# Optimization experiments

Hardware: AMD Instinct MI355X
Metric: run time of the kernel (lower is better)

Reference implementation:

```python
import jax, jax.numpy as jnp
import numpy as np

EMBED = 1024
HEADS = 16
HEAD_DIM = EMBED // HEADS
HIDDEN = 4 * EMBED
EPS = 1e-5


def layer_norm(x, g, b):
    mu = jnp.mean(x, axis=-1, keepdims=True)
    var = jnp.var(x, axis=-1, keepdims=True)
    return (x - mu) * jax.lax.rsqrt(var + EPS) * g + b


def setup_inputs() -> dict:
    key = jax.random.key(0)
    ks = jax.random.split(key, 12)
    s_e = 1.0 / np.sqrt(EMBED)
    s_h = 1.0 / np.sqrt(HIDDEN)
    return {
        "x": jax.random.normal(ks[0], (8, 1024, EMBED), dtype=jnp.float32),
        "ln1_g": jnp.ones((EMBED,), jnp.float32),
        "ln1_b": jnp.zeros((EMBED,), jnp.float32),
        "w_qkv": jax.random.normal(ks[1], (EMBED, 3 * EMBED), jnp.float32) * s_e,
        "b_qkv": jax.random.normal(ks[2], (3 * EMBED,), jnp.float32) * s_e,
        "w_out": jax.random.normal(ks[3], (EMBED, EMBED), jnp.float32) * s_e,
        "b_out": jax.random.normal(ks[4], (EMBED,), jnp.float32) * s_e,
        "ln2_g": jnp.ones((EMBED,), jnp.float32),
        "ln2_b": jnp.zeros((EMBED,), jnp.float32),
        "w_up": jax.random.normal(ks[5], (EMBED, HIDDEN), jnp.float32) * s_e,
        "b_up": jax.random.normal(ks[6], (HIDDEN,), jnp.float32) * s_e,
        "w_down": jax.random.normal(ks[7], (HIDDEN, EMBED), jnp.float32) * s_h,
        "b_down": jax.random.normal(ks[8], (EMBED,), jnp.float32) * s_h,
    }


def reference(x, ln1_g, ln1_b, w_qkv, b_qkv, w_out, b_out,
              ln2_g, ln2_b, w_up, b_up, w_down, b_down):
    B, T, C = x.shape
    # --- attention sub-block ---
    h = layer_norm(x, ln1_g, ln1_b)
    qkv = h @ w_qkv + b_qkv                                   # [B,T,3C]
    q, k, v = jnp.split(qkv, 3, axis=-1)
    def heads(t):  # [B,T,C] -> [B,H,T,D]
        return t.reshape(B, T, HEADS, HEAD_DIM).transpose(0, 2, 1, 3)
    q, k, v = heads(q), heads(k), heads(v)
    scale = HEAD_DIM ** -0.5
    attn = jax.nn.softmax(jnp.einsum('bhqd,bhkd->bhqk', q, k) * scale, axis=-1)
    y = jnp.einsum('bhqk,bhkd->bhqd', attn, v)                # [B,H,T,D]
    y = y.transpose(0, 2, 1, 3).reshape(B, T, C)
    x = x + y @ w_out + b_out
    # --- MLP sub-block ---
    h = layer_norm(x, ln2_g, ln2_b)
    h = jax.nn.relu(h @ w_up + b_up)
    x = x + h @ w_down + b_down
    return x
```

## Files before the change

kernel.cpp:

```cpp
#include <hip/hip_runtime.h>
#include <stdint.h>


typedef __attribute__((ext_vector_type(8))) short short8;
typedef __attribute__((ext_vector_type(4))) short short4v;
typedef __attribute__((ext_vector_type(4))) float floatx4;

#define NROWS 8192

__device__ __forceinline__ unsigned short f2bf(float f) {
    union { float f; unsigned u; } x; x.f = f;
    unsigned r = x.u + 0x7fffu + ((x.u >> 16) & 1u);
    return (unsigned short)(r >> 16);
}

__device__ __forceinline__ void gl2lds16(const unsigned short* g, unsigned short* l) {
    __builtin_amdgcn_global_load_lds(
        (const __attribute__((address_space(1))) unsigned int*)(uintptr_t)g,
        (__attribute__((address_space(3))) unsigned int*)(unsigned int)(uintptr_t)l,
        16, 0, 0);
}

__global__ __launch_bounds__(256) void transpose_bf16(
    const float* __restrict__ in, unsigned short* __restrict__ out, int K, int N)
{
    __shared__ unsigned short tile[32][33];
    int n0 = blockIdx.x * 32, k0 = blockIdx.y * 32;
    int tx = threadIdx.x, ty = threadIdx.y;
    #pragma unroll
    for (int i = 0; i < 4; ++i)
        tile[ty + i * 8][tx] = f2bf(in[(size_t)(k0 + ty + i * 8) * N + n0 + tx]);
    __syncthreads();
    #pragma unroll
    for (int i = 0; i < 4; ++i)
        out[(size_t)(n0 + ty + i * 8) * K + k0 + tx] = tile[tx][ty + i * 8];
}

__global__ __launch_bounds__(256) void ln_bf16(
    const float* __restrict__ x, const float* __restrict__ g,
    const float* __restrict__ b, unsigned short* __restrict__ out)
{
    int row = blockIdx.x, t = threadIdx.x;
    const float4* xr = (const float4*)(x + (size_t)row * 1024);
    float4 v = xr[t];
    float s  = v.x + v.y + v.z + v.w;
    float s2 = v.x * v.x + v.y * v.y + v.z * v.z + v.w * v.w;
    #pragma unroll
    for (int off = 32; off; off >>= 1) {
        s  += __shfl_xor(s,  off, 64);
        s2 += __shfl_xor(s2, off, 64);
    }
    __shared__ float rs[4], rs2[4];
    int w = t >> 6;
    if ((t & 63) == 0) { rs[w] = s; rs2[w] = s2; }
    __syncthreads();
    s  = rs[0] + rs[1] + rs[2] + rs[3];
    s2 = rs2[0] + rs2[1] + rs2[2] + rs2[3];
    float mean = s * (1.0f / 1024.0f);
    float var  = s2 * (1.0f / 1024.0f) - mean * mean;
    float rstd = rsqrtf(var + 1e-5f);
    float4 gv = ((const float4*)g)[t];
    float4 bv = ((const float4*)b)[t];
    ushort4 o;
    o.x = f2bf((v.x - mean) * rstd * gv.x + bv.x);
    o.y = f2bf((v.y - mean) * rstd * gv.y + bv.y);
    o.z = f2bf((v.z - mean) * rstd * gv.z + bv.z);
    o.w = f2bf((v.w - mean) * rstd * gv.w + bv.w);
    ((ushort4*)(out + (size_t)row * 1024))[t] = o;
}

template <int MODE, int TN>
__global__ __launch_bounds__(256, 2) void gemm_mfma(
    const unsigned short* __restrict__ A, const unsigned short* __restrict__ Bt,
    int M, int N, int K,
    const float* __restrict__ bias, const float* __restrict__ resid,
    float* __restrict__ outF, unsigned short* __restrict__ outB,
    unsigned short* __restrict__ qO, unsigned short* __restrict__ kO,
    unsigned short* __restrict__ vO)
{
    constexpr int NJ  = TN / 32;
    constexpr int TNH = TN / 2;
    int m0 = blockIdx.x * 128, n0 = blockIdx.y * TN;
    int tid = threadIdx.x;
    int w = tid >> 6, l = tid & 63, quad = l >> 4, lr = l & 15;
    int wm = w & 1, wn = w >> 1;

    __shared__ unsigned short As[128 * 32];
    __shared__ unsigned short Bs[TN * 32];

    floatx4 acc[4][NJ];
    #pragma unroll
    for (int i = 0; i < 4; ++i)
        #pragma unroll
        for (int j = 0; j < NJ; ++j)
            acc[i][j] = (floatx4){0.f, 0.f, 0.f, 0.f};

    int srow = l >> 2;
    int scol = (l & 3) * 8;
    const unsigned short* Ag = A  + (size_t)(m0 + w * 32 + srow) * K + scol;
    const unsigned short* Bg = Bt + (size_t)(n0 + w * (TN / 4) + srow) * K + scol;
    unsigned short* As0 = &As[(w * 32) * 32];
    unsigned short* As1 = &As[(w * 32 + 16) * 32];
    unsigned short* Bsw = &Bs[(w * (TN / 4)) * 32];

    for (int kt = 0; kt < K; kt += 32) {
        gl2lds16(Ag + kt, As0);
        gl2lds16(Ag + (size_t)16 * K + kt, As1);
        #pragma unroll
        for (int u = 0; u < TN / 64; ++u)
            gl2lds16(Bg + (size_t)(16 * u) * K + kt, Bsw + (16 * u) * 32);
        __syncthreads();
        short8 af[4], bf[NJ];
        #pragma unroll
        for (int i = 0; i < 4; ++i)
            af[i] = *(const short8*)&As[(64 * wm + 16 * i + lr) * 32 + quad * 8];
        #pragma unroll
        for (int j = 0; j < NJ; ++j)
            bf[j] = *(const short8*)&Bs[(TNH * wn + 16 * j + lr) * 32 + quad * 8];
        #pragma unroll
        for (int i = 0; i < 4; ++i)
            #pragma unroll
            for (int j = 0; j < NJ; ++j)
                acc[i][j] = __builtin_amdgcn_mfma_f32_16x16x32_bf16(
                    af[i], bf[j], acc[i][j], 0, 0, 0);
        __syncthreads();
    }

    if (MODE == 0) {
        int sel = n0 >> 10;
        if (sel < 2) {
            const float qscale = (sel == 0) ? 0.125f : 1.0f;
            unsigned short* dst = (sel == 0) ? qO : kO;
            #pragma unroll
            for (int i = 0; i < 4; ++i)
                #pragma unroll
                for (int j = 0; j < NJ; ++j)
                    #pragma unroll
                    for (int r = 0; r < 4; ++r) {
                        int m = m0 + 64 * wm + 16 * i + quad * 4 + r;
                        int n = n0 + TNH * wn + 16 * j + lr;
                        float c = (acc[i][j][r] + bias[n]) * qscale;
                        int bb = m >> 10, t = m & 1023;
                        int cc = n & 1023, h = cc >> 6, d = cc & 63;
                        dst[(((size_t)(bb * 16 + h)) * 1024 + t) * 64 + d] = f2bf(c);
                    }
        } else {
            int bb = m0 >> 10;
            #pragma unroll
            for (int i = 0; i < 4; ++i) {
                int t0 = (m0 & 1023) + 64 * wm + 16 * i + quad * 4;
                #pragma unroll
                for (int j = 0; j < NJ; ++j) {
                    int n = n0 + TNH * wn + 16 * j + lr;
                    int cc = n & 1023, h = cc >> 6, d = cc & 63;
                    float bn = bias[n];
                    ushort4 pk;
                    pk.x = f2bf(acc[i][j][0] + bn);
                    pk.y = f2bf(acc[i][j][1] + bn);
                    pk.z = f2bf(acc[i][j][2] + bn);
                    pk.w = f2bf(acc[i][j][3] + bn);
                    *(ushort4*)&vO[((size_t)(bb * 16 + h) * 64 + d) * 1024 + t0] = pk;
                }
            }
        }
    } else {
        #pragma unroll
        for (int i = 0; i < 4; ++i)
            #pragma unroll
            for (int j = 0; j < NJ; ++j)
                #pragma unroll
                for (int r = 0; r < 4; ++r) {
                    int m = m0 + 64 * wm + 16 * i + quad * 4 + r;
                    int n = n0 + TNH * wn + 16 * j + lr;
                    float c = acc[i][j][r] + bias[n];
                    if (MODE == 1)
                        outF[(size_t)m * N + n] = c + resid[(size_t)m * N + n];
                    else
                        outB[(size_t)m * N + n] = f2bf(fmaxf(c, 0.f));
                }
    }
}

__global__ __launch_bounds__(256, 2) void attn_kernel(
    const unsigned short* __restrict__ qg, const unsigned short* __restrict__ kg,
    const unsigned short* __restrict__ vtg, unsigned short* __restrict__ y)
{
    int bid = blockIdx.x;
    int bh = bid & 127, qt = bid >> 7;
    int b = bh >> 4, h = bh & 15;
    int tid = threadIdx.x;
    int w = tid >> 6, l = tid & 63, quad = l >> 4, lr = l & 15;

    __shared__ unsigned short Qs[128 * 64];
    __shared__ unsigned short Ks[2][64 * 64];
    __shared__ unsigned short Vs[2][64 * 64];
    __shared__ unsigned short Ps[4][32 * 68];

    int srow = l >> 3;
    int scol = ((l & 7) ^ srow) * 8;

    {
        const unsigned short* qbase = qg + (size_t)bh * 65536 + (size_t)(qt * 128) * 64;
        #pragma unroll
        for (int u = 0; u < 4; ++u)
            gl2lds16(qbase + (size_t)(32 * w + 8 * u + srow) * 64 + scol,
                     &Qs[(32 * w + 8 * u) * 64]);
    }
    const unsigned short* kbase = kg  + (size_t)bh * 65536;
    const unsigned short* vbase = vtg + (size_t)bh * 65536;

    #pragma unroll
    for (int u = 0; u < 2; ++u) {
        gl2lds16(kbase + (size_t)(16 * w + 8 * u + srow) * 64 + scol,
                 &Ks[0][(16 * w + 8 * u) * 64]);
        gl2lds16(vbase + (size_t)(16 * w + 8 * u + srow) * 1024 + scol,
                 &Vs[0][(16 * w + 8 * u) * 64]);
    }
    __syncthreads();

    short8 af[2][2];
    #pragma unroll
    for (int i = 0; i < 2; ++i)
        #pragma unroll
        for (int s = 0; s < 2; ++s)
            af[i][s] = *(const short8*)
                &Qs[(32 * w + 16 * i + lr) * 64 + ((s * 4 + quad) ^ (lr & 7)) * 8];

    floatx4 o[2][4];
    float lsum[2][4];
    #pragma unroll
    for (int i = 0; i < 2; ++i)
        #pragma unroll
        for (int j = 0; j < 4; ++j) o[i][j] = (floatx4){0.f, 0.f, 0.f, 0.f};
    #pragma unroll
    for (int i = 0; i < 2; ++i)
        #pragma unroll
        for (int r = 0; r < 4; ++r) lsum[i][r] = 0.f;

    for (int kt = 0; kt < 16; ++kt) {
        int cur = kt & 1;
        if (kt + 1 < 16) {
            const unsigned short* kb = kbase + (size_t)((kt + 1) * 64) * 64;
            const unsigned short* vb = vbase + (size_t)((kt + 1) * 64);
            #pragma unroll
            for (int u = 0; u < 2; ++u) {
                gl2lds16(kb + (size_t)(16 * w + 8 * u + srow) * 64 + scol,
                         &Ks[cur ^ 1][(16 * w + 8 * u) * 64]);
                gl2lds16(vb + (size_t)(16 * w + 8 * u + srow) * 1024 + scol,
                         &Vs[cur ^ 1][(16 * w + 8 * u) * 64]);
            }
        }

        short8 kf[4][2];
        #pragma unroll
        for (int j = 0; j < 4; ++j)
            #pragma unroll
            for (int s = 0; s < 2; ++s)
                kf[j][s] = *(const short8*)
                    &Ks[cur][(16 * j + lr) * 64 + ((s * 4 + quad) ^ (lr & 7)) * 8];

        floatx4 s[2][4];
        #pragma unroll
        for (int i = 0; i < 2; ++i)
            #pragma unroll
            for (int j = 0; j < 4; ++j) {
                s[i][j] = (floatx4){0.f, 0.f, 0.f, 0.f};
                #pragma unroll
                for (int st = 0; st < 2; ++st)
                    s[i][j] = __builtin_amdgcn_mfma_f32_16x16x32_bf16(
                        af[i][st], kf[j][st], s[i][j], 0, 0, 0);
            }

        #pragma unroll
        for (int i = 0; i < 2; ++i)
            #pragma unroll
            for (int j = 0; j < 4; ++j)
                #pragma unroll
                for (int r = 0; r < 4; ++r) {
                    float p = __expf(s[i][j][r]);
                    lsum[i][r] += p;
                    Ps[w][(16 * i + quad * 4 + r) * 68 + 16 * j + lr] = f2bf(p);
                }

        asm volatile("s_waitcnt lgkmcnt(0)" ::: "memory");

        short8 vf[4][2];
        #pragma unroll
        for (int j = 0; j < 4; ++j)
            #pragma unroll
            for (int s = 0; s < 2; ++s)
                vf[j][s] = *(const short8*)
                    &Vs[cur][(16 * j + lr) * 64 + ((s * 4 + quad) ^ (lr & 7)) * 8];

        #pragma unroll
        for (int i = 0; i < 2; ++i)
            #pragma unroll
            for (int st = 0; st < 2; ++st) {
                short4v p0 = *(const short4v*)&Ps[w][(16 * i + lr) * 68 + st * 32 + quad * 8];
                short4v p1 = *(const short4v*)&Ps[w][(16 * i + lr) * 68 + st * 32 + quad * 8 + 4];
                short8 pf;
                #pragma unroll
                for (int e = 0; e < 4; ++e) { pf[e] = p0[e]; pf[e + 4] = p1[e]; }
                #pragma unroll
                for (int j = 0; j < 4; ++j)
                    o[i][j] = __builtin_amdgcn_mfma_f32_16x16x32_bf16(
                        pf, vf[j][st], o[i][j], 0, 0, 0);
            }
        __syncthreads();
    }

    #pragma unroll
    for (int off = 8; off; off >>= 1)
        #pragma unroll
        for (int i = 0; i < 2; ++i)
            #pragma unroll
            for (int r = 0; r < 4; ++r)
                lsum[i][r] += __shfl_xor(lsum[i][r], off, 64);
    float rinv[2][4];
    #pragma unroll
    for (int i = 0; i < 2; ++i)
        #pragma unroll
        for (int r = 0; r < 4; ++r) rinv[i][r] = 1.0f / lsum[i][r];

    #pragma unroll
    for (int i = 0; i < 2; ++i)
        #pragma unroll
        for (int j = 0; j < 4; ++j)
            #pragma unroll
            for (int r = 0; r < 4; ++r) {
                int trow = qt * 128 + 32 * w + 16 * i + quad * 4 + r;
                int col  = h * 64 + 16 * j + lr;
                y[((size_t)b * 1024 + trow) * 1024 + col] =
                    f2bf(o[i][j][r] * rinv[i][r]);
            }
}

extern "C" void kernel_launch(void* const* d_in, const int* in_sizes, int n_in,
                              void* d_out, int out_size, void* d_ws, size_t ws_size,
                              hipStream_t stream)
{
    const float* x      = (const float*)d_in[0];
    const float* ln1_g  = (const float*)d_in[1];
    const float* ln1_b  = (const float*)d_in[2];
    const float* w_qkv  = (const float*)d_in[3];
    const float* b_qkv  = (const float*)d_in[4];
    const float* w_out  = (const float*)d_in[5];
    const float* b_out  = (const float*)d_in[6];
    const float* ln2_g  = (const float*)d_in[7];
    const float* ln2_b  = (const float*)d_in[8];
    const float* w_up   = (const float*)d_in[9];
    const float* b_up   = (const float*)d_in[10];
    const float* w_down = (const float*)d_in[11];
    const float* b_down = (const float*)d_in[12];

    char* ws = (char*)d_ws;
    unsigned short* wqkvT  = (unsigned short*)(ws + 0);
    unsigned short* woutT  = (unsigned short*)(ws + 6291456);
    unsigned short* wupT   = (unsigned short*)(ws + 8388608);
    unsigned short* wdownT = (unsigned short*)(ws + 16777216);
    float*          x2     = (float*)(ws + 25165824);
    unsigned short* h1     = (unsigned short*)(ws + 58720256);
    unsigned short* qb     = (unsigned short*)(ws + 75497472);
    unsigned short* kb     = (unsigned short*)(ws + 92274688);
    unsigned short* vtb    = (unsigned short*)(ws + 109051904);
    unsigned short* yb     = (unsigned short*)(ws + 125829120);
    unsigned short* a2     = (unsigned short*)(ws + 75497472);
    unsigned short* h2     = h1;

    transpose_bf16<<<dim3(3072 / 32, 1024 / 32), dim3(32, 8), 0, stream>>>(w_qkv, wqkvT, 1024, 3072);
    transpose_bf16<<<dim3(1024 / 32, 1024 / 32), dim3(32, 8), 0, stream>>>(w_out, woutT, 1024, 1024);
    transpose_bf16<<<dim3(4096 / 32, 1024 / 32), dim3(32, 8), 0, stream>>>(w_up,  wupT,  1024, 4096);
    transpose_bf16<<<dim3(1024 / 32, 4096 / 32), dim3(32, 8), 0, stream>>>(w_down, wdownT, 4096, 1024);

    ln_bf16<<<NROWS, 256, 0, stream>>>(x, ln1_g, ln1_b, h1);

    gemm_mfma<0, 256><<<dim3(NROWS / 128, 3072 / 256), 256, 0, stream>>>(
        h1, wqkvT, NROWS, 3072, 1024, b_qkv, nullptr, nullptr, nullptr, qb, kb, vtb);

    attn_kernel<<<1024, 256, 0, stream>>>(qb, kb, vtb, yb);

    gemm_mfma<1, 128><<<dim3(NROWS / 128, 1024 / 128), 256, 0, stream>>>(
        yb, woutT, NROWS, 1024, 1024, b_out, x, x2, nullptr, nullptr, nullptr, nullptr);

    ln_bf16<<<NROWS, 256, 0, stream>>>(x2, ln2_g, ln2_b, h2);

    gemm_mfma<2, 256><<<dim3(NROWS / 128, 4096 / 256), 256, 0, stream>>>(
        h2, wupT, NROWS, 4096, 1024, b_up, nullptr, nullptr, a2, nullptr, nullptr, nullptr);

    gemm_mfma<1, 128><<<dim3(NROWS / 128, 1024 / 128), 256, 0, stream>>>(
        a2, wdownT, NROWS, 1024, 4096, b_down, x2, (float*)d_out, nullptr, nullptr, nullptr, nullptr);
}
```

Measured before the change: 490.4 us.

## Add double-buffered swizzled-LDS GEMM for residual projections

Adds a new gemm_dbuf kernel for the out-projection and down-projection GEMMs. It uses K-tiles of 64, double-buffered LDS so the next tile's global-to-LDS loads overlap MFMA work, and an XOR swizzle on LDS columns to avoid bank conflicts. There is one barrier per iteration instead of two. The LDS footprint grows to 64KB per block, which may limit occupancy. The old templated GEMM is specialised to TN=256 for the QKV and up projections.

```diff
diff --git a/kernel.cpp b/kernel.cpp
--- a/kernel.cpp
+++ b/kernel.cpp
@@ -69,17 +69,98 @@
     ((ushort4*)(out + (size_t)row * 1024))[t] = o;
 }
 
-template <int MODE, int TN>
+__global__ __launch_bounds__(256, 2) void gemm_dbuf(
+    const unsigned short* __restrict__ A, const unsigned short* __restrict__ Bt,
+    int M, int N, int K,
+    const float* __restrict__ bias, const float* __restrict__ resid,
+    float* __restrict__ outF)
+{
+    int m0 = blockIdx.x * 128, n0 = blockIdx.y * 128;
+    int tid = threadIdx.x;
+    int w = tid >> 6, l = tid & 63, quad = l >> 4, lr = l & 15;
+    int wm = w & 1, wn = w >> 1;
+
+    __shared__ unsigned short As[2][128 * 64];
+    __shared__ unsigned short Bs[2][128 * 64];
+
+    floatx4 acc[4][4];
+    #pragma unroll
+    for (int i = 0; i < 4; ++i)
+        #pragma unroll
+        for (int j = 0; j < 4; ++j)
+            acc[i][j] = (floatx4){0.f, 0.f, 0.f, 0.f};
+
+    int srow = l >> 3;
+    int scol = ((l & 7) ^ srow) * 8;
+    const unsigned short* Ag = A  + (size_t)(m0 + 32 * w + srow) * K + scol;
+    const unsigned short* Bg = Bt + (size_t)(n0 + 32 * w + srow) * K + scol;
+
+    #pragma unroll
+    for (int u = 0; u < 4; ++u) {
+        gl2lds16(Ag + (size_t)(8 * u) * K, &As[0][(32 * w + 8 * u) * 64]);
+        gl2lds16(Bg + (size_t)(8 * u) * K, &Bs[0][(32 * w + 8 * u) * 64]);
+    }
+    __syncthreads();
+
+    for (int kt = 0; kt < K; kt += 64) {
+        int cur = (kt >> 6) & 1;
+        if (kt + 64 < K) {
+            #pragma unroll
+            for (int u = 0; u < 4; ++u) {
+                gl2lds16(Ag + (size_t)(8 * u) * K + kt + 64,
+                         &As[cur ^ 1][(32 * w + 8 * u) * 64]);
+                gl2lds16(Bg + (size_t)(8 * u) * K + kt + 64,
+                         &Bs[cur ^ 1][(32 * w + 8 * u) * 64]);
+            }
+        }
+        short8 af[4][2], bf[4][2];
+        #pragma unroll
+        for (int i = 0; i < 4; ++i)
+            #pragma unroll
+            for (int s = 0; s < 2; ++s)
+                af[i][s] = *(const short8*)
+                    &As[cur][(64 * wm + 16 * i + lr) * 64 + (((s * 4 + quad) ^ (lr & 7)) * 8)];
+        #pragma unroll
+        for (int j = 0; j < 4; ++j)
+            #pragma unroll
+            for (int s = 0; s < 2; ++s)
+                bf[j][s] = *(const short8*)
+                    &Bs[cur][(64 * wn + 16 * j + lr) * 64 + (((s * 4 + quad) ^ (lr & 7)) * 8)];
+        #pragma unroll
+        for (int i = 0; i < 4; ++i)
+            #pragma unroll
+            for (int j = 0; j < 4; ++j) {
+                acc[i][j] = __builtin_amdgcn_mfma_f32_16x16x32_bf16(
+                    af[i][0], bf[j][0], acc[i][j], 0, 0, 0);
+                acc[i][j] = __builtin_amdgcn_mfma_f32_16x16x32_bf16(
+                    af[i][1], bf[j][1], acc[i][j], 0, 0, 0);
+            }
+        __syncthreads();
+    }
+
+    #pragma unroll
+    for (int i = 0; i < 4; ++i)
+        #pragma unroll
+        for (int j = 0; j < 4; ++j)
+            #pragma unroll
+            for (int r = 0; r < 4; ++r) {
+                int m = m0 + 64 * wm + 16 * i + quad * 4 + r;
+                int n = n0 + 64 * wn + 16 * j + lr;
+                outF[(size_t)m * N + n] =
+                    acc[i][j][r] + bias[n] + resid[(size_t)m * N + n];
+            }
+}
+
+template <int MODE>
 __global__ __launch_bounds__(256, 2) void gemm_mfma(
     const unsigned short* __restrict__ A, const unsigned short* __restrict__ Bt,
     int M, int N, int K,
-    const float* __restrict__ bias, const float* __restrict__ resid,
-    float* __restrict__ outF, unsigned short* __restrict__ outB,
+    const float* __restrict__ bias,
+    unsigned short* __restrict__ outB,
     unsigned short* __restrict__ qO, unsigned short* __restrict__ kO,
     unsigned short* __restrict__ vO)
 {
-    constexpr int NJ  = TN / 32;
-    constexpr int TNH = TN / 2;
+    constexpr int TN = 256, NJ = 8, TNH = 128;
     int m0 = blockIdx.x * 128, n0 = blockIdx.y * TN;
     int tid = threadIdx.x;
     int w = tid >> 6, l = tid & 63, quad = l >> 4, lr = l & 15;
@@ -98,16 +179,16 @@
     int srow = l >> 2;
     int scol = (l & 3) * 8;
     const unsigned short* Ag = A  + (size_t)(m0 + w * 32 + srow) * K + scol;
-    const unsigned short* Bg = Bt + (size_t)(n0 + w * (TN / 4) + srow) * K + scol;
+    const unsigned short* Bg = Bt + (size_t)(n0 + w * 64 + srow) * K + scol;
     unsigned short* As0 = &As[(w * 32) * 32];
     unsigned short* As1 = &As[(w * 32 + 16) * 32];
-    unsigned short* Bsw = &Bs[(w * (TN / 4)) * 32];
+    unsigned short* Bsw = &Bs[(w * 64) * 32];
 
     for (int kt = 0; kt < K; kt += 32) {
         gl2lds16(Ag + kt, As0);
         gl2lds16(Ag + (size_t)16 * K + kt, As1);
         #pragma unroll
-        for (int u = 0; u < TN / 64; ++u)
+        for (int u = 0; u < 4; ++u)
             gl2lds16(Bg + (size_t)(16 * u) * K + kt, Bsw + (16 * u) * 32);
         __syncthreads();
         short8 af[4], bf[NJ];
@@ -172,11 +253,7 @@
                 for (int r = 0; r < 4; ++r) {
                     int m = m0 + 64 * wm + 16 * i + quad * 4 + r;
                     int n = n0 + TNH * wn + 16 * j + lr;
-                    float c = acc[i][j][r] + bias[n];
-                    if (MODE == 1)
-                        outF[(size_t)m * N + n] = c + resid[(size_t)m * N + n];
-                    else
-                        outB[(size_t)m * N + n] = f2bf(fmaxf(c, 0.f));
+                    outB[(size_t)m * N + n] = f2bf(fmaxf(acc[i][j][r] + bias[n], 0.f));
                 }
     }
 }
@@ -374,19 +451,19 @@
 
     ln_bf16<<<NROWS, 256, 0, stream>>>(x, ln1_g, ln1_b, h1);
 
-    gemm_mfma<0, 256><<<dim3(NROWS / 128, 3072 / 256), 256, 0, stream>>>(
-        h1, wqkvT, NROWS, 3072, 1024, b_qkv, nullptr, nullptr, nullptr, qb, kb, vtb);
+    gemm_mfma<0><<<dim3(NROWS / 128, 3072 / 256), 256, 0, stream>>>(
+        h1, wqkvT, NROWS, 3072, 1024, b_qkv, nullptr, qb, kb, vtb);
 
     attn_kernel<<<1024, 256, 0, stream>>>(qb, kb, vtb, yb);
 
-    gemm_mfma<1, 128><<<dim3(NROWS / 128, 1024 / 128), 256, 0, stream>>>(
-        yb, woutT, NROWS, 1024, 1024, b_out, x, x2, nullptr, nullptr, nullptr, nullptr);
+    gemm_dbuf<<<dim3(NROWS / 128, 1024 / 128), 256, 0, stream>>>(
+        yb, woutT, NROWS, 1024, 1024, b_out, x, x2);
 
     ln_bf16<<<NROWS, 256, 0, stream>>>(x2, ln2_g, ln2_b, h2);
 
-    gemm_mfma<2, 256><<<dim3(NROWS / 128, 4096 / 256), 256, 0, stream>>>(
-        h2, wupT, NROWS, 4096, 1024, b_up, nullptr, nullptr, a2, nullptr, nullptr, nullptr);
-
-    gemm_mfma<1, 128><<<dim3(NROWS / 128, 1024 / 128), 256, 0, stream>>>(
-        a2, wdownT, NROWS, 1024, 4096, b_down, x2, (float*)d_out, nullptr, nullptr, nullptr, nullptr);
-}
+    gemm_mfma<2><<<dim3(NROWS / 128, 4096 / 256), 256, 0, stream>>>(
+        h2, wupT, NROWS, 4096, 1024, b_up, a2, nullptr, nullptr, nullptr);
+
+    gemm_dbuf<<<dim3(NROWS / 128, 1024 / 128), 256, 0, stream>>>(
+        a2, wdownT, NROWS, 1024, 4096, b_down, x2, (float*)d_out);
+}
```

Result: faster. 474.2 us (-3.3%).
